# Optimization experiments

Measured on AMD Instinct MI355X. Metric: run time of the kernel, lower is better.

Reference implementation:

```python
import jax, jax.numpy as jnp
import numpy as np

C = 64  # in_dim

def _dwpw(x, w_dw, w_pw):
    # depthwise 1x1x1 conv (groups=C, no bias) == per-channel scale
    x = x * w_dw[None, :, None, None, None]
    # pointwise 1x1x1 conv (no bias) == channel mixing matmul
    return jnp.einsum('bcdhw,oc->bodhw', x, w_pw)

def setup_inputs() -> dict:
    key = jax.random.key(0)
    ks = jax.random.split(key, 8)
    B, D, H, W = 2, 16, 16, 16
    x = jax.random.normal(ks[0], (B, C, D, H, W), dtype=jnp.float32)
    s = 1.0 / np.sqrt(C)
    q_dw = jax.random.normal(ks[1], (C,), dtype=jnp.float32) * s
    q_pw = jax.random.normal(ks[2], (C, C), dtype=jnp.float32) * s
    k_dw = jax.random.normal(ks[3], (C,), dtype=jnp.float32) * s
    k_pw = jax.random.normal(ks[4], (C, C), dtype=jnp.float32) * s
    v_dw = jax.random.normal(ks[5], (C,), dtype=jnp.float32) * s
    v_pw = jax.random.normal(ks[6], (C, C), dtype=jnp.float32) * s
    gamma = jnp.zeros((1,), dtype=jnp.float32) + 0.1  # nonzero so output depends on attention
    return {"x": x, "q_dw": q_dw, "q_pw": q_pw, "k_dw": k_dw, "k_pw": k_pw,
            "v_dw": v_dw, "v_pw": v_pw, "gamma": gamma}

def reference(x, q_dw, q_pw, k_dw, k_pw, v_dw, v_pw, gamma):
    B, Cc, D, H, W = x.shape
    N = D * H * W
    q = _dwpw(x, q_dw, q_pw).reshape(B, Cc, N)  # [B,C,N]
    k = _dwpw(x, k_dw, k_pw).reshape(B, Cc, N)
    v = _dwpw(x, v_dw, v_pw).reshape(B, Cc, N)
    # energy[b,i,j] = sum_c q[b,c,i] * k[b,c,j]
    energy = jnp.einsum('bci,bcj->bij', q, k)
    attn = jax.nn.softmax(energy, axis=-1)  # softmax over j
    # out[b,c,i] = sum_j v[b,c,j] * attn[b,i,j]
    out = jnp.einsum('bcj,bij->bci', v, attn).reshape(B, Cc, D, H, W)
    return gamma * out + x
```

## Files before the change

kernel.cpp:

```cpp
#include <hip/hip_runtime.h>
#include <hip/hip_bf16.h>

#define NPOS 4096
#define CDIM 64
#define BATCH 2
#define JSPLIT 16
#define JCHUNK (NPOS / JSPLIT)
#define RPB 128
#define PSTR 72

typedef __attribute__((ext_vector_type(8))) short bf16x8;
typedef __attribute__((ext_vector_type(4))) short short4b;
typedef __attribute__((ext_vector_type(4))) float f32x4;
typedef __attribute__((ext_vector_type(4))) unsigned int u32x4;
typedef __attribute__((ext_vector_type(2))) unsigned int u32x2;

static __device__ __forceinline__ unsigned int fbits(float f) {
    union { float f; unsigned int u; } v; v.f = f; return v.u;
}
static __device__ __forceinline__ float bffloat(unsigned int hi16) {
    union { unsigned int u; float f; } v; v.u = hi16; return v.f;
}
static __device__ __forceinline__ unsigned int pk2bf(float a, float b) {
    return ((fbits(a) + 0x8000u) >> 16) | ((fbits(b) + 0x8000u) & 0xffff0000u);
}
static __device__ __forceinline__ short f2bs(float f) {
    return (short)(unsigned short)((fbits(f) + 0x8000u) >> 16);
}

__global__ __launch_bounds__(64) void qkv_kernel(
    const float* __restrict__ x,
    const float* __restrict__ q_dw, const float* __restrict__ q_pw,
    const float* __restrict__ k_dw, const float* __restrict__ k_pw,
    const float* __restrict__ v_dw, const float* __restrict__ v_pw,
    short* __restrict__ qT, short* __restrict__ kT, short* __restrict__ vM)
{
    const int bid  = blockIdx.x;
    const int p    = bid >> 9;
    const int np   = bid & 511;
    const int b    = np >> 8;
    const int n0   = (np & 255) << 4;
    const int lane = threadIdx.x;
    const int col  = lane & 15;
    const int quad = lane >> 4;
    const int n    = n0 + col;

    const float* pw = (p == 0) ? q_pw : (p == 1) ? k_pw : v_pw;
    const float* dw = (p == 0) ? q_dw : (p == 1) ? k_dw : v_dw;

    bf16x8 xf0, xf1;
    float dv0[8], dv1[8];
    #pragma unroll
    for (int j = 0; j < 8; ++j) {
        xf0[j] = f2bs(x[(size_t)(b * CDIM + quad * 8 + j) * NPOS + n]);
        xf1[j] = f2bs(x[(size_t)(b * CDIM + 32 + quad * 8 + j) * NPOS + n]);
        dv0[j] = dw[quad * 8 + j];
        dv1[j] = dw[32 + quad * 8 + j];
    }

    #pragma unroll
    for (int os = 0; os < 4; ++os) {
        const float* pr = pw + (os * 16 + col) * 64 + quad * 8;
        bf16x8 wf0, wf1;
        #pragma unroll
        for (int j = 0; j < 8; ++j) {
            wf0[j] = f2bs(pr[j] * dv0[j]);
            wf1[j] = f2bs(pr[32 + j] * dv1[j]);
        }
        f32x4 d = (f32x4){0.f, 0.f, 0.f, 0.f};
        if (p < 2) {
            d = __builtin_amdgcn_mfma_f32_16x16x32_bf16(wf0, xf0, d, 0, 0, 0);
            d = __builtin_amdgcn_mfma_f32_16x16x32_bf16(wf1, xf1, d, 0, 0, 0);
            short* dst = p ? kT : qT;
            *(u32x2*)(dst + (size_t)(b * NPOS + n) * CDIM + os * 16 + quad * 4) =
                (u32x2){pk2bf(d[0], d[1]), pk2bf(d[2], d[3])};
        } else {
            d = __builtin_amdgcn_mfma_f32_16x16x32_bf16(xf0, wf0, d, 0, 0, 0);
            d = __builtin_amdgcn_mfma_f32_16x16x32_bf16(xf1, wf1, d, 0, 0, 0);
            *(u32x2*)(vM + (size_t)(b * CDIM + os * 16 + col) * NPOS + n0 + quad * 4) =
                (u32x2){pk2bf(d[0], d[1]), pk2bf(d[2], d[3])};
        }
    }
}

__global__ __launch_bounds__(256, 3) void attn_kernel(
    const short* __restrict__ qT, const short* __restrict__ kT,
    const short* __restrict__ vM,
    unsigned short* __restrict__ Opart, float* __restrict__ lacc)
{
    const int gid  = blockIdx.x;
    const int jc   = gid & (JSPLIT - 1);
    const int rb   = (gid >> 4) & 31;
    const int b    = gid >> 9;
    const int t    = threadIdx.x;
    const int wave = t >> 6;
    const int lane = t & 63;
    const int col  = lane & 15;
    const int quad = lane >> 4;

    __shared__ __align__(16) short Pw[4][32 * PSTR];

    const short* qTb = qT + (size_t)b * NPOS * CDIM;
    const short* kTb = kT + (size_t)b * NPOS * CDIM;
    const short* vb  = vM + (size_t)b * CDIM * NPOS;

    const int i0 = rb * RPB + wave * 32;

    bf16x8 qf[2][2];
    #pragma unroll
    for (int rs = 0; rs < 2; ++rs) {
        const short* qp = qTb + (size_t)(i0 + rs * 16 + col) * CDIM + quad * 8;
        qf[rs][0] = *(const bf16x8*)qp;
        qf[rs][1] = *(const bf16x8*)(qp + 32);
    }

    f32x4 oacc[2][4];
    #pragma unroll
    for (int rs = 0; rs < 2; ++rs)
        #pragma unroll
        for (int cb = 0; cb < 4; ++cb) oacc[rs][cb] = (f32x4){0.f, 0.f, 0.f, 0.f};
    float lp[2] = {0.f, 0.f};

    short* Pme = Pw[wave];

    #pragma unroll
    for (int jt = 0; jt < JCHUNK / 64; ++jt) {
        const int j0 = jc * JCHUNK + jt * 64;

        bf16x8 kf[4][2], vf[4][2];
        #pragma unroll
        for (int ct = 0; ct < 4; ++ct) {
            const short* kp = kTb + (size_t)(j0 + ct * 16 + col) * CDIM + quad * 8;
            kf[ct][0] = *(const bf16x8*)kp;
            kf[ct][1] = *(const bf16x8*)(kp + 32);
        }
        #pragma unroll
        for (int cb = 0; cb < 4; ++cb) {
            const short* vp = vb + (size_t)(cb * 16 + col) * NPOS + j0 + quad * 8;
            vf[cb][0] = *(const bf16x8*)vp;
            vf[cb][1] = *(const bf16x8*)(vp + 32);
        }

        #pragma unroll
        for (int ct = 0; ct < 4; ++ct) {
            #pragma unroll
            for (int rs = 0; rs < 2; ++rs) {
                f32x4 a = (f32x4){0.f, 0.f, 0.f, 0.f};
                a = __builtin_amdgcn_mfma_f32_16x16x32_bf16(kf[ct][0], qf[rs][0], a, 0, 0, 0);
                a = __builtin_amdgcn_mfma_f32_16x16x32_bf16(kf[ct][1], qf[rs][1], a, 0, 0, 0);
                float p0 = __expf(a[0]), p1 = __expf(a[1]);
                float p2 = __expf(a[2]), p3 = __expf(a[3]);
                lp[rs] += (p0 + p1) + (p2 + p3);
                *(short4b*)(Pme + (rs * 16 + col) * PSTR + ct * 16 + quad * 4) =
                    (short4b){f2bs(p0), f2bs(p1), f2bs(p2), f2bs(p3)};
            }
        }

        bf16x8 pf[2][2];
        #pragma unroll
        for (int rs = 0; rs < 2; ++rs) {
            const short* pp = Pme + (rs * 16 + col) * PSTR + quad * 8;
            pf[rs][0] = *(const bf16x8*)pp;
            pf[rs][1] = *(const bf16x8*)(pp + 32);
        }

        #pragma unroll
        for (int cb = 0; cb < 4; ++cb)
            #pragma unroll
            for (int rs = 0; rs < 2; ++rs) {
                oacc[rs][cb] = __builtin_amdgcn_mfma_f32_16x16x32_bf16(vf[cb][0], pf[rs][0], oacc[rs][cb], 0, 0, 0);
                oacc[rs][cb] = __builtin_amdgcn_mfma_f32_16x16x32_bf16(vf[cb][1], pf[rs][1], oacc[rs][cb], 0, 0, 0);
            }
    }

    #pragma unroll
    for (int rs = 0; rs < 2; ++rs) {
        lp[rs] += __shfl_xor(lp[rs], 16, 64);
        lp[rs] += __shfl_xor(lp[rs], 32, 64);
    }
    if (quad == 0) {
        #pragma unroll
        for (int rs = 0; rs < 2; ++rs)
            lacc[(size_t)(jc * BATCH + b) * NPOS + i0 + rs * 16 + col] = lp[rs];
    }

    unsigned short* Ob = Opart + (size_t)(jc * BATCH + b) * CDIM * NPOS;
    #pragma unroll
    for (int rs = 0; rs < 2; ++rs)
        #pragma unroll
        for (int cb = 0; cb < 4; ++cb)
            #pragma unroll
            for (int r = 0; r < 4; ++r)
                Ob[(size_t)(cb * 16 + quad * 4 + r) * NPOS + i0 + rs * 16 + col] =
                    (unsigned short)f2bs(oacc[rs][cb][r]);
}

__global__ __launch_bounds__(256) void combine_kernel(
    const unsigned short* __restrict__ Opart, const float* __restrict__ lacc,
    const float* __restrict__ x, const float* __restrict__ gamma,
    float* __restrict__ out)
{
    int b  = blockIdx.x >> 7;
    int n0 = (blockIdx.x & 127) << 5;
    __shared__ float linv[32];
    int t = threadIdx.x;
    if (t < 32) {
        float s = 0.f;
        #pragma unroll
        for (int jc = 0; jc < JSPLIT; ++jc)
            s += lacc[(size_t)(jc * BATCH + b) * NPOS + n0 + t];
        linv[t] = gamma[0] / s;
    }
    __syncthreads();

    int c = t >> 2, ns = (t & 3) * 8;
    float acc[8];
    #pragma unroll
    for (int k = 0; k < 8; ++k) acc[k] = 0.f;
    #pragma unroll
    for (int jc = 0; jc < JSPLIT; ++jc) {
        const unsigned short* Ob = Opart + ((size_t)(jc * BATCH + b) * CDIM + c) * NPOS + n0 + ns;
        u32x4 w = *(const u32x4*)Ob;
        #pragma unroll
        for (int j = 0; j < 4; ++j) {
            acc[2 * j]     += bffloat(w[j] << 16);
            acc[2 * j + 1] += bffloat(w[j] & 0xffff0000u);
        }
    }
    const float* xb = x + ((size_t)b * CDIM + c) * NPOS + n0 + ns;
    float* ob = out + ((size_t)b * CDIM + c) * NPOS + n0 + ns;
    #pragma unroll
    for (int k = 0; k < 2; ++k) {
        f32x4 x4 = *(const f32x4*)(xb + k * 4);
        f32x4 r;
        #pragma unroll
        for (int j = 0; j < 4; ++j)
            r[j] = fmaf(acc[k * 4 + j], linv[ns + k * 4 + j], x4[j]);
        *(f32x4*)(ob + k * 4) = r;
    }
}

extern "C" void kernel_launch(void* const* d_in, const int* in_sizes, int n_in,
                              void* d_out, int out_size, void* d_ws, size_t ws_size,
                              hipStream_t stream) {
    const float* x     = (const float*)d_in[0];
    const float* q_dw  = (const float*)d_in[1];
    const float* q_pw  = (const float*)d_in[2];
    const float* k_dw  = (const float*)d_in[3];
    const float* k_pw  = (const float*)d_in[4];
    const float* v_dw  = (const float*)d_in[5];
    const float* v_pw  = (const float*)d_in[6];
    const float* gamma = (const float*)d_in[7];
    float* out = (float*)d_out;

    char* ws = (char*)d_ws;
    short* qT             = (short*)(ws);
    short* kT             = (short*)(ws + (1u << 20));
    short* vM             = (short*)(ws + (2u << 20));
    unsigned short* Opart = (unsigned short*)(ws + (3u << 20));
    float* lacc           = (float*)(ws + (3u << 20) +
                                     (size_t)JSPLIT * BATCH * CDIM * NPOS * 2);

    qkv_kernel<<<3 * BATCH * 256, 64, 0, stream>>>(
        x, q_dw, q_pw, k_dw, k_pw, v_dw, v_pw, qT, kT, vM);
    attn_kernel<<<BATCH * 32 * JSPLIT, 256, 0, stream>>>(qT, kT, vM, Opart, lacc);
    combine_kernel<<<BATCH * 128, 256, 0, stream>>>(Opart, lacc, x, gamma, out);
}
```

Before: 118.4 us.

## Stage K/V tiles in double-buffered swizzled LDS via async global-to-LDS loads

The attention kernel now loads each 64-position K and V tile once per block into double-buffered shared memory using global_load_lds with an XOR swizzle. Previously each of the four waves fetched the same tiles from global memory on its own. The next tile is prefetched while the current one is computed, and a block barrier separates iterations. The J split is halved from 16 to 8, so each block processes more tiles and the grid is smaller, and the launch-bounds occupancy hint drops from 3 to 2 to fit the larger LDS footprint. The cost is extra barriers and fewer blocks in flight, which may underfill the GPU.

Result: faster. 97.54 us (-17.6%).

```diff
diff --git a/kernel.cpp b/kernel.cpp
--- a/kernel.cpp
+++ b/kernel.cpp
@@ -4,8 +4,10 @@
 #define NPOS 4096
 #define CDIM 64
 #define BATCH 2
-#define JSPLIT 16
+#define JSPLIT 8
+#define JSHIFT 3
 #define JCHUNK (NPOS / JSPLIT)
+#define NTILE (JCHUNK / 64)
 #define RPB 128
 #define PSTR 72
 
@@ -26,6 +28,12 @@
 }
 static __device__ __forceinline__ short f2bs(float f) {
     return (short)(unsigned short)((fbits(f) + 0x8000u) >> 16);
+}
+
+static __device__ __forceinline__ void gload16(const void* g, void* l) {
+    __builtin_amdgcn_global_load_lds(
+        (const __attribute__((address_space(1))) unsigned int*)g,
+        (__attribute__((address_space(3))) unsigned int*)l, 16, 0, 0);
 }
 
 __global__ __launch_bounds__(64) void qkv_kernel(
@@ -83,28 +91,47 @@
     }
 }
 
-__global__ __launch_bounds__(256, 3) void attn_kernel(
+__global__ __launch_bounds__(256, 2) void attn_kernel(
     const short* __restrict__ qT, const short* __restrict__ kT,
     const short* __restrict__ vM,
     unsigned short* __restrict__ Opart, float* __restrict__ lacc)
 {
     const int gid  = blockIdx.x;
     const int jc   = gid & (JSPLIT - 1);
-    const int rb   = (gid >> 4) & 31;
-    const int b    = gid >> 9;
+    const int rb   = (gid >> JSHIFT) & 31;
+    const int b    = gid >> (JSHIFT + 5);
     const int t    = threadIdx.x;
     const int wave = t >> 6;
     const int lane = t & 63;
     const int col  = lane & 15;
     const int quad = lane >> 4;
 
+    __shared__ __align__(16) short Kbuf[2][64 * 64];
+    __shared__ __align__(16) short Vbuf[2][64 * 64];
     __shared__ __align__(16) short Pw[4][32 * PSTR];
 
     const short* qTb = qT + (size_t)b * NPOS * CDIM;
-    const short* kTb = kT + (size_t)b * NPOS * CDIM;
-    const short* vb  = vM + (size_t)b * CDIM * NPOS;
+    const char*  kTB = (const char*)(kT + (size_t)b * NPOS * CDIM);
+    const char*  vB  = (const char*)(vM + (size_t)b * CDIM * NPOS);
 
     const int i0 = rb * RPB + wave * 32;
+
+    auto stage = [&](int tt) {
+        const int j0 = jc * JCHUNK + tt * 64;
+        const char* kS = kTB + (size_t)j0 * (CDIM * 2);
+        const char* vS = vB  + (size_t)j0 * 2;
+        char* kD = (char*)&Kbuf[tt & 1][0];
+        char* vD = (char*)&Vbuf[tt & 1][0];
+        #pragma unroll
+        for (int i = 0; i < 2; ++i) {
+            const int base = wave * 2048 + i * 1024;
+            const int L    = base + lane * 16;
+            const int r    = L >> 7;
+            const int o    = (L & 127) ^ ((r & 7) << 4);
+            gload16(kS + (size_t)((L & ~127) + o), kD + base);
+            gload16(vS + (size_t)r * (NPOS * 2) + o, vD + base);
+        }
+    };
 
     bf16x8 qf[2][2];
     #pragma unroll
@@ -122,32 +149,27 @@
     float lp[2] = {0.f, 0.f};
 
     short* Pme = Pw[wave];
-
-    #pragma unroll
-    for (int jt = 0; jt < JCHUNK / 64; ++jt) {
-        const int j0 = jc * JCHUNK + jt * 64;
-
-        bf16x8 kf[4][2], vf[4][2];
+    const int slot = (quad * 16) ^ ((col & 7) << 4);
+
+    stage(0);
+    __syncthreads();
+
+    for (int tt = 0; tt < NTILE; ++tt) {
+        if (tt + 1 < NTILE) stage(tt + 1);
+
+        const char* Kc = (const char*)&Kbuf[tt & 1][0];
+        const char* Vc = (const char*)&Vbuf[tt & 1][0];
+
         #pragma unroll
         for (int ct = 0; ct < 4; ++ct) {
-            const short* kp = kTb + (size_t)(j0 + ct * 16 + col) * CDIM + quad * 8;
-            kf[ct][0] = *(const bf16x8*)kp;
-            kf[ct][1] = *(const bf16x8*)(kp + 32);
-        }
-        #pragma unroll
-        for (int cb = 0; cb < 4; ++cb) {
-            const short* vp = vb + (size_t)(cb * 16 + col) * NPOS + j0 + quad * 8;
-            vf[cb][0] = *(const bf16x8*)vp;
-            vf[cb][1] = *(const bf16x8*)(vp + 32);
-        }
-
-        #pragma unroll
-        for (int ct = 0; ct < 4; ++ct) {
+            const char* kr = Kc + (ct * 16 + col) * 128;
+            bf16x8 k0 = *(const bf16x8*)(kr + slot);
+            bf16x8 k1 = *(const bf16x8*)(kr + (slot ^ 64));
             #pragma unroll
             for (int rs = 0; rs < 2; ++rs) {
                 f32x4 a = (f32x4){0.f, 0.f, 0.f, 0.f};
-                a = __builtin_amdgcn_mfma_f32_16x16x32_bf16(kf[ct][0], qf[rs][0], a, 0, 0, 0);
-                a = __builtin_amdgcn_mfma_f32_16x16x32_bf16(kf[ct][1], qf[rs][1], a, 0, 0, 0);
+                a = __builtin_amdgcn_mfma_f32_16x16x32_bf16(k0, qf[rs][0], a, 0, 0, 0);
+                a = __builtin_amdgcn_mfma_f32_16x16x32_bf16(k1, qf[rs][1], a, 0, 0, 0);
                 float p0 = __expf(a[0]), p1 = __expf(a[1]);
                 float p2 = __expf(a[2]), p3 = __expf(a[3]);
                 lp[rs] += (p0 + p1) + (p2 + p3);
@@ -165,12 +187,17 @@
         }
 
         #pragma unroll
-        for (int cb = 0; cb < 4; ++cb)
+        for (int cb = 0; cb < 4; ++cb) {
+            const char* vr = Vc + (cb * 16 + col) * 128;
+            bf16x8 v0 = *(const bf16x8*)(vr + slot);
+            bf16x8 v1 = *(const bf16x8*)(vr + (slot ^ 64));
             #pragma unroll
             for (int rs = 0; rs < 2; ++rs) {
-                oacc[rs][cb] = __builtin_amdgcn_mfma_f32_16x16x32_bf16(vf[cb][0], pf[rs][0], oacc[rs][cb], 0, 0, 0);
-                oacc[rs][cb] = __builtin_amdgcn_mfma_f32_16x16x32_bf16(vf[cb][1], pf[rs][1], oacc[rs][cb], 0, 0, 0);
+                oacc[rs][cb] = __builtin_amdgcn_mfma_f32_16x16x32_bf16(v0, pf[rs][0], oacc[rs][cb], 0, 0, 0);
+                oacc[rs][cb] = __builtin_amdgcn_mfma_f32_16x16x32_bf16(v1, pf[rs][1], oacc[rs][cb], 0, 0, 0);
             }
+        }
+        __syncthreads();
     }
 
     #pragma unroll
```
